# Kernel tuning notes

Measured on AMD Instinct MI355X. Metric: run time of the kernel, lower is better.

## Reference

```python
import jax, jax.numpy as jnp
import numpy as np

B = 32768
INPUT_DIM = 2048
D = 2
HIDDEN = 128
V = 20          # output_dim (number of heads)
P = 6           # n_corr_params
R = 10          # r_lora = min(V // 2, 10)


def setup_inputs() -> dict:
    key = jax.random.key(0)
    ks = jax.random.split(key, 12)

    def lin(k, fan_in, shape):
        bound = 1.0 / np.sqrt(fan_in)
        return jax.random.uniform(k, shape, jnp.float32, -bound, bound)

    x = jax.random.normal(ks[0], (B, INPUT_DIM), jnp.float32)
    # encoder: Linear(input_dim, hidden) -> ReLU -> (Dropout=id) -> Linear(hidden, d)
    We1 = lin(ks[1], INPUT_DIM, (INPUT_DIM, HIDDEN))
    be1 = lin(ks[2], INPUT_DIM, (HIDDEN,))
    We2 = lin(ks[3], HIDDEN, (HIDDEN, D))
    be2 = lin(ks[4], HIDDEN, (D,))
    # 20 heads, each Linear(d, hidden) -> ReLU -> Linear(hidden, 6) -> Tanh,
    # stacked into batched weight tensors.
    W1 = lin(ks[5], D, (V, D, HIDDEN))
    b1 = lin(ks[6], D, (V, HIDDEN))
    W2 = lin(ks[7], HIDDEN, (V, HIDDEN, P))
    b2 = lin(ks[8], HIDDEN, (V, P))
    # LoRA params
    lora_A = jax.random.normal(ks[9], (D, R), jnp.float32) * 0.01
    lora_B = jax.random.normal(ks[10], (R, V * P), jnp.float32) * 0.01
    return {"x": x, "We1": We1, "be1": be1, "We2": We2, "be2": be2,
            "W1": W1, "b1": b1, "W2": W2, "b2": b2,
            "lora_A": lora_A, "lora_B": lora_B}


def reference(x, We1, be1, We2, be2, W1, b1, W2, b2, lora_A, lora_B):
    # encoder (nonlinear reduction; dropout is identity in eval)
    z = jax.nn.relu(x @ We1 + be1) @ We2 + be2            # [B, D]
    # all 20 heads as batched GEMMs
    h = jax.nn.relu(jnp.einsum('bd,vdh->bvh', z, W1) + b1)  # [B, V, HIDDEN]
    heads = jnp.tanh(jnp.einsum('bvh,vhp->bvp', h, W2) + b2)  # [B, V, P]
    # LoRA contribution, then outer tanh (note: double tanh, faithful to source)
    lora = (z @ lora_A @ lora_B).reshape(-1, V, P)         # [B, V, P]
    out = jnp.tanh(heads + 0.15 * lora)
    return (out, z)
```

## Files before the change

### kernel.cpp

```cpp
#include <hip/hip_runtime.h>
#include <hip/hip_bf16.h>
#include <cstdint>
#include <cstddef>

#define BDIM   32768
#define KDIM   2048
#define NDIM   128
#define VHEADS 20
#define PDIM   6
#define RLORA  10

#define BK      64
#define NCHUNK  (KDIM / BK)
#define OUT_ELEMS   (BDIM * VHEADS * PDIM)
#define WS_W_BYTES  (KDIM * NDIM * 2)

typedef __attribute__((ext_vector_type(8))) __bf16 bf16x8;
typedef __attribute__((ext_vector_type(4))) float f32x4;
typedef __attribute__((ext_vector_type(2))) float f32x2;
typedef __attribute__((ext_vector_type(4))) unsigned int u32x4;

union FragU { bf16x8 b; u32x4 u; };

__device__ __forceinline__ unsigned int cvt_pk_bf16(float lo, float hi) {
  unsigned int r;
  asm("v_cvt_pk_bf16_f32 %0, %1, %2" : "=v"(r) : "v"(lo), "v"(hi));
  return r;
}

__device__ __forceinline__ void gload_lds16(const void* g, void* l) {
  __builtin_amdgcn_global_load_lds(
      (const __attribute__((address_space(1))) void*)(g),
      (__attribute__((address_space(3))) void*)(l), 16, 0, 0);
}

__device__ __forceinline__ float fast_tanh(float x) {
  float ax = fabsf(x);
  float e  = __expf(-2.0f * ax);
  float t  = __fdividef(1.0f - e, 1.0f + e);
  return copysignf(t, x);
}

#define SBAR() __builtin_amdgcn_sched_barrier(0)

__global__ __launch_bounds__(256)
void k0_pack(const float* __restrict__ We1,
             const float* __restrict__ lA,
             const float* __restrict__ lB,
             unsigned short* __restrict__ wsw,
             float* __restrict__ wsM) {
  if (blockIdx.x == 128) {
    int t = threadIdx.x;
    if (t < 2 * VHEADS * PDIM) {
      int d  = t / (VHEADS * PDIM);
      int vp = t - d * (VHEADS * PDIM);
      float s = 0.f;
#pragma unroll
      for (int r = 0; r < RLORA; ++r)
        s = fmaf(lA[d * RLORA + r], lB[r * (VHEADS * PDIM) + vp], s);
      wsM[t] = s;
    }
    return;
  }
  int t    = blockIdx.x * 256 + threadIdx.x;
  int lane = t & 63;
  int blk  = t >> 6;
  int ks   = blk & 1;
  int nt   = (blk >> 1) & 7;
  int c    = blk >> 4;
  int n    = nt * 16 + (lane & 15);
  int kb   = c * 64 + ks * 32 + (lane >> 4) * 8;

  unsigned int u[4];
#pragma unroll
  for (int q = 0; q < 4; ++q) {
    float f0 = We1[(size_t)(kb + 2 * q + 0) * NDIM + n];
    float f1 = We1[(size_t)(kb + 2 * q + 1) * NDIM + n];
    __hip_bfloat16 h0 = __float2bfloat16(f0);
    __hip_bfloat16 h1 = __float2bfloat16(f1);
    u[q] = (unsigned int)*reinterpret_cast<unsigned short*>(&h0) |
           ((unsigned int)*reinterpret_cast<unsigned short*>(&h1) << 16);
  }
  *reinterpret_cast<u32x4*>(wsw + (size_t)t * 8) = u32x4{u[0], u[1], u[2], u[3]};
}

__global__ __launch_bounds__(512, 4)
void k1_fused(const float* __restrict__ x,
              const unsigned short* __restrict__ wp,
              const float* __restrict__ be1,
              const float* __restrict__ We2,
              const float* __restrict__ be2,
              const float* __restrict__ W1,
              const float* __restrict__ b1,
              const float* __restrict__ W2,
              const float* __restrict__ b2,
              const float* __restrict__ M,
              float* __restrict__ out,
              float* __restrict__ zout) {
  __shared__ char A0_[16384] __attribute__((aligned(16)));
  __shared__ char A1_[16384] __attribute__((aligned(16)));
  __shared__ char B0_[16384] __attribute__((aligned(16)));
  __shared__ char B1_[16384] __attribute__((aligned(16)));
  __shared__ float zpart2[64][2][2];
  __shared__ float zsh[64][2];

  const int tid  = threadIdx.x;
  const int lane = tid & 63;
  const int wv   = tid >> 6;
  const int wr   = wv & 3;
  const int wc   = wv >> 2;
  const int l15  = lane & 15;
  const int kgrp = lane >> 4;
  const int blk  = blockIdx.x;

  f32x4 acc[4];
#pragma unroll
  for (int i = 0; i < 4; ++i) acc[i] = f32x4{0.f, 0.f, 0.f, 0.f};

  auto STAGE = [&](char* Ad, char* Bd, int c) {
#pragma unroll
    for (int q = 0; q < 2; ++q) {
      int s = tid + q * 512;
      int row = s >> 4;
      int g = (s & 15) ^ (row & 7);
      const float* asrc = x + (size_t)(blk * 64 + row) * KDIM + c * BK + g * 4;
      gload_lds16(asrc, Ad + s * 16);
    }
#pragma unroll
    for (int q = 0; q < 2; ++q) {
      gload_lds16((const char*)wp + (size_t)c * 16384 + q * 8192 + tid * 16,
                  Bd + q * 8192 + tid * 16);
    }
  };

  auto COMPUTE = [&](const char* Ad, const char* Bd) {
    const int row = wr * 16 + l15;
    const char* abase = Ad + row * 256;
    const int rx = (row & 7) << 4;
    f32x4 A0 = *(const f32x4*)(abase + (((kgrp * 2 + 0) << 4) ^ rx));
    f32x4 A1 = *(const f32x4*)(abase + (((kgrp * 2 + 1) << 4) ^ rx));
    f32x4 A2 = *(const f32x4*)(abase + 128 + (((kgrp * 2 + 0) << 4) ^ rx));
    f32x4 A3 = *(const f32x4*)(abase + 128 + (((kgrp * 2 + 1) << 4) ^ rx));
    FragU a0, a1;
    a0.u = u32x4{cvt_pk_bf16(A0.x, A0.y), cvt_pk_bf16(A0.z, A0.w),
                 cvt_pk_bf16(A1.x, A1.y), cvt_pk_bf16(A1.z, A1.w)};
    a1.u = u32x4{cvt_pk_bf16(A2.x, A2.y), cvt_pk_bf16(A2.z, A2.w),
                 cvt_pk_bf16(A3.x, A3.y), cvt_pk_bf16(A3.z, A3.w)};
    const char* bbase = Bd + lane * 16;
#pragma unroll
    for (int nt = 0; nt < 4; ++nt) {
      FragU b0, b1;
      b0.u = *(const u32x4*)(bbase + ((wc * 4 + nt) * 2 + 0) * 1024);
      b1.u = *(const u32x4*)(bbase + ((wc * 4 + nt) * 2 + 1) * 1024);
      acc[nt] = __builtin_amdgcn_mfma_f32_16x16x32_bf16(a0.b, b0.b, acc[nt], 0, 0, 0);
      acc[nt] = __builtin_amdgcn_mfma_f32_16x16x32_bf16(a1.b, b1.b, acc[nt], 0, 0, 0);
    }
  };

  STAGE(A0_, B0_, 0);
  STAGE(A1_, B1_, 1);

#pragma unroll 1
  for (int cc = 0; cc < NCHUNK / 2 - 1; ++cc) {
    asm volatile("s_waitcnt vmcnt(4)" ::: "memory");
    SBAR();
    __builtin_amdgcn_s_barrier();
    COMPUTE(A0_, B0_);
    __builtin_amdgcn_s_barrier();
    SBAR();
    STAGE(A0_, B0_, 2 * cc + 2);
    asm volatile("s_waitcnt vmcnt(4)" ::: "memory");
    SBAR();
    __builtin_amdgcn_s_barrier();
    COMPUTE(A1_, B1_);
    __builtin_amdgcn_s_barrier();
    SBAR();
    STAGE(A1_, B1_, 2 * cc + 3);
  }
  asm volatile("s_waitcnt vmcnt(4)" ::: "memory");
  SBAR();
  __builtin_amdgcn_s_barrier();
  COMPUTE(A0_, B0_);
  asm volatile("s_waitcnt vmcnt(0)" ::: "memory");
  SBAR();
  __builtin_amdgcn_s_barrier();
  COMPUTE(A1_, B1_);

  float part[4][2];
#pragma unroll
  for (int j = 0; j < 4; ++j) { part[j][0] = 0.f; part[j][1] = 0.f; }
#pragma unroll
  for (int nt = 0; nt < 4; ++nt) {
    int col = (wc * 4 + nt) * 16 + l15;
    float bb = be1[col];
    float w0 = We2[col * 2 + 0];
    float w1 = We2[col * 2 + 1];
#pragma unroll
    for (int j = 0; j < 4; ++j) {
      float h = acc[nt][j] + bb;
      h = h > 0.f ? h : 0.f;
      part[j][0] = fmaf(h, w0, part[j][0]);
      part[j][1] = fmaf(h, w1, part[j][1]);
    }
  }
#pragma unroll
  for (int m = 1; m < 16; m <<= 1) {
#pragma unroll
    for (int j = 0; j < 4; ++j) {
      part[j][0] += __shfl_xor(part[j][0], m, 64);
      part[j][1] += __shfl_xor(part[j][1], m, 64);
    }
  }
  if (l15 == 0) {
#pragma unroll
    for (int j = 0; j < 4; ++j) {
      int rl = wr * 16 + kgrp * 4 + j;
      zpart2[rl][wc][0] = part[j][0];
      zpart2[rl][wc][1] = part[j][1];
    }
  }
  __syncthreads();
  if (tid < 64) {
    float s0 = zpart2[tid][0][0] + zpart2[tid][1][0] + be2[0];
    float s1 = zpart2[tid][0][1] + zpart2[tid][1][1] + be2[1];
    zsh[tid][0] = s0;
    zsh[tid][1] = s1;
    f32x2 zz = {s0, s1};
    *(f32x2*)(zout + (size_t)(blk * 64 + tid) * 2) = zz;
  }
  __syncthreads();

  const int wvu = __builtin_amdgcn_readfirstlane(wv);
  float z0 = zsh[lane][0];
  float z1 = zsh[lane][1];
  float* orow = out + (size_t)(blk * 64 + lane) * (VHEADS * PDIM);

  auto head = [&](int v) {
    const float* w1a = W1 + (size_t)(v * 2 + 0) * NDIM;
    const float* w1b = W1 + (size_t)(v * 2 + 1) * NDIM;
    const float* bb1 = b1 + (size_t)v * NDIM;
    const float* w2  = W2 + (size_t)v * NDIM * PDIM;

    float p[6] = {0.f, 0.f, 0.f, 0.f, 0.f, 0.f};
#pragma unroll 4
    for (int h = 0; h < NDIM; ++h) {
      float hv = fmaf(z0, w1a[h], fmaf(z1, w1b[h], bb1[h]));
      hv = hv > 0.f ? hv : 0.f;
#pragma unroll
      for (int j = 0; j < 6; ++j) p[j] = fmaf(hv, w2[h * 6 + j], p[j]);
    }
    float o[6];
#pragma unroll
    for (int j = 0; j < 6; ++j) {
      float t1 = fast_tanh(p[j] + b2[v * PDIM + j]);
      float lo = fmaf(z0, M[v * PDIM + j], z1 * M[VHEADS * PDIM + v * PDIM + j]);
      o[j] = fast_tanh(fmaf(0.15f, lo, t1));
    }
    float* op = orow + v * PDIM;
    f32x2 o01 = {o[0], o[1]};
    f32x2 o23 = {o[2], o[3]};
    f32x2 o45 = {o[4], o[5]};
    __builtin_nontemporal_store(o01, (f32x2*)(op + 0));
    __builtin_nontemporal_store(o23, (f32x2*)(op + 2));
    __builtin_nontemporal_store(o45, (f32x2*)(op + 4));
  };

  head(wvu);
  head(wvu + 8);
  if (wvu < 4) head(wvu + 16);
}

extern "C" void kernel_launch(void* const* d_in, const int* in_sizes, int n_in,
                              void* d_out, int out_size, void* d_ws, size_t ws_size,
                              hipStream_t stream) {
  const float* x   = (const float*)d_in[0];
  const float* We1 = (const float*)d_in[1];
  const float* be1 = (const float*)d_in[2];
  const float* We2 = (const float*)d_in[3];
  const float* be2 = (const float*)d_in[4];
  const float* W1  = (const float*)d_in[5];
  const float* b1  = (const float*)d_in[6];
  const float* W2  = (const float*)d_in[7];
  const float* b2  = (const float*)d_in[8];
  const float* lA  = (const float*)d_in[9];
  const float* lB  = (const float*)d_in[10];

  float* out  = (float*)d_out;
  float* zout = out + OUT_ELEMS;
  unsigned short* wsw = (unsigned short*)d_ws;
  float* wsM = (float*)((char*)d_ws + WS_W_BYTES);

  hipLaunchKernelGGL(k0_pack, dim3(129), dim3(256), 0, stream,
                     We1, lA, lB, wsw, wsM);
  hipLaunchKernelGGL(k1_fused, dim3(BDIM / 64), dim3(512), 0, stream,
                     x, wsw, be1, We2, be2, W1, b1, W2, b2, wsM, out, zout);
}
```

Before: 95.87 us.

## Load packed weight fragments directly into registers instead of staging through LDS

The bf16 weight tile is no longer staged through shared memory. Each wave now loads its B fragments straight from global memory into double-buffered registers with inline-asm dwordx4 loads, and the vmcnt waits are adjusted to match. This removes the LDS round trip and halves LDS usage, which could allow more resident blocks. In exchange each wave separately re-fetches B that was previously shared across the block, register pressure rises, and correctness depends on hand-counted vmcnt values with inline asm the compiler cannot track.

```diff
diff --git a/kernel.cpp b/kernel.cpp
--- a/kernel.cpp
+++ b/kernel.cpp
@@ -42,6 +42,9 @@
 }
 
 #define SBAR() __builtin_amdgcn_sched_barrier(0)
+#define GL16(dst, addr, OFFSTR) \
+  asm volatile("global_load_dwordx4 %0, %1, off offset:" OFFSTR \
+               : "=v"(dst) : "v"(addr))
 
 __global__ __launch_bounds__(256)
 void k0_pack(const float* __restrict__ We1,
@@ -99,8 +102,6 @@
               float* __restrict__ zout) {
   __shared__ char A0_[16384] __attribute__((aligned(16)));
   __shared__ char A1_[16384] __attribute__((aligned(16)));
-  __shared__ char B0_[16384] __attribute__((aligned(16)));
-  __shared__ char B1_[16384] __attribute__((aligned(16)));
   __shared__ float zpart2[64][2][2];
   __shared__ float zsh[64][2];
 
@@ -113,11 +114,13 @@
   const int kgrp = lane >> 4;
   const int blk  = blockIdx.x;
 
+  const char* bwave = (const char*)wp + wc * 8192 + lane * 16 + 4096;
+
   f32x4 acc[4];
 #pragma unroll
   for (int i = 0; i < 4; ++i) acc[i] = f32x4{0.f, 0.f, 0.f, 0.f};
 
-  auto STAGE = [&](char* Ad, char* Bd, int c) {
+  auto STAGE_A = [&](char* Ad, int c) {
 #pragma unroll
     for (int q = 0; q < 2; ++q) {
       int s = tid + q * 512;
@@ -126,14 +129,22 @@
       const float* asrc = x + (size_t)(blk * 64 + row) * KDIM + c * BK + g * 4;
       gload_lds16(asrc, Ad + s * 16);
     }
-#pragma unroll
-    for (int q = 0; q < 2; ++q) {
-      gload_lds16((const char*)wp + (size_t)c * 16384 + q * 8192 + tid * 16,
-                  Bd + q * 8192 + tid * 16);
-    }
   };
 
-  auto COMPUTE = [&](const char* Ad, const char* Bd) {
+  FragU bE[8], bO[8];
+  auto LOADB = [&](FragU* B, int c) {
+    const char* p = bwave + (size_t)c * 16384;
+    GL16(B[0].u, p, "-4096");
+    GL16(B[1].u, p, "-3072");
+    GL16(B[2].u, p, "-2048");
+    GL16(B[3].u, p, "-1024");
+    GL16(B[4].u, p, "0");
+    GL16(B[5].u, p, "1024");
+    GL16(B[6].u, p, "2048");
+    GL16(B[7].u, p, "3072");
+  };
+
+  auto COMPUTE = [&](const char* Ad, const FragU* B) {
     const int row = wr * 16 + l15;
     const char* abase = Ad + row * 256;
     const int rx = (row & 7) << 4;
@@ -146,45 +157,48 @@
                  cvt_pk_bf16(A1.x, A1.y), cvt_pk_bf16(A1.z, A1.w)};
     a1.u = u32x4{cvt_pk_bf16(A2.x, A2.y), cvt_pk_bf16(A2.z, A2.w),
                  cvt_pk_bf16(A3.x, A3.y), cvt_pk_bf16(A3.z, A3.w)};
-    const char* bbase = Bd + lane * 16;
-#pragma unroll
-    for (int nt = 0; nt < 4; ++nt) {
-      FragU b0, b1;
-      b0.u = *(const u32x4*)(bbase + ((wc * 4 + nt) * 2 + 0) * 1024);
-      b1.u = *(const u32x4*)(bbase + ((wc * 4 + nt) * 2 + 1) * 1024);
-      acc[nt] = __builtin_amdgcn_mfma_f32_16x16x32_bf16(a0.b, b0.b, acc[nt], 0, 0, 0);
-      acc[nt] = __builtin_amdgcn_mfma_f32_16x16x32_bf16(a1.b, b1.b, acc[nt], 0, 0, 0);
-    }
+    acc[0] = __builtin_amdgcn_mfma_f32_16x16x32_bf16(a0.b, B[0].b, acc[0], 0, 0, 0);
+    acc[0] = __builtin_amdgcn_mfma_f32_16x16x32_bf16(a1.b, B[1].b, acc[0], 0, 0, 0);
+    acc[1] = __builtin_amdgcn_mfma_f32_16x16x32_bf16(a0.b, B[2].b, acc[1], 0, 0, 0);
+    acc[1] = __builtin_amdgcn_mfma_f32_16x16x32_bf16(a1.b, B[3].b, acc[1], 0, 0, 0);
+    acc[2] = __builtin_amdgcn_mfma_f32_16x16x32_bf16(a0.b, B[4].b, acc[2], 0, 0, 0);
+    acc[2] = __builtin_amdgcn_mfma_f32_16x16x32_bf16(a1.b, B[5].b, acc[2], 0, 0, 0);
+    acc[3] = __builtin_amdgcn_mfma_f32_16x16x32_bf16(a0.b, B[6].b, acc[3], 0, 0, 0);
+    acc[3] = __builtin_amdgcn_mfma_f32_16x16x32_bf16(a1.b, B[7].b, acc[3], 0, 0, 0);
   };
 
-  STAGE(A0_, B0_, 0);
-  STAGE(A1_, B1_, 1);
+  STAGE_A(A0_, 0);
+  LOADB(bE, 0);
+  STAGE_A(A1_, 1);
+  LOADB(bO, 1);
 
 #pragma unroll 1
   for (int cc = 0; cc < NCHUNK / 2 - 1; ++cc) {
-    asm volatile("s_waitcnt vmcnt(4)" ::: "memory");
+    asm volatile("s_waitcnt vmcnt(10)" ::: "memory");
     SBAR();
     __builtin_amdgcn_s_barrier();
-    COMPUTE(A0_, B0_);
+    COMPUTE(A0_, bE);
     __builtin_amdgcn_s_barrier();
     SBAR();
-    STAGE(A0_, B0_, 2 * cc + 2);
-    asm volatile("s_waitcnt vmcnt(4)" ::: "memory");
+    STAGE_A(A0_, 2 * cc + 2);
+    LOADB(bE, 2 * cc + 2);
+    asm volatile("s_waitcnt vmcnt(10)" ::: "memory");
     SBAR();
     __builtin_amdgcn_s_barrier();
-    COMPUTE(A1_, B1_);
+    COMPUTE(A1_, bO);
     __builtin_amdgcn_s_barrier();
     SBAR();
-    STAGE(A1_, B1_, 2 * cc + 3);
-  }
-  asm volatile("s_waitcnt vmcnt(4)" ::: "memory");
+    STAGE_A(A1_, 2 * cc + 3);
+    LOADB(bO, 2 * cc + 3);
+  }
+  asm volatile("s_waitcnt vmcnt(10)" ::: "memory");
   SBAR();
   __builtin_amdgcn_s_barrier();
-  COMPUTE(A0_, B0_);
+  COMPUTE(A0_, bE);
   asm volatile("s_waitcnt vmcnt(0)" ::: "memory");
   SBAR();
   __builtin_amdgcn_s_barrier();
-  COMPUTE(A1_, B1_);
+  COMPUTE(A1_, bO);
 
   float part[4][2];
 #pragma unroll
```

Measured after the change: 99.55 us. 1.04x slower.

## Enlarge row tile to 128 with 1024-thread blocks and single-buffered B

Applied to the files above, without the earlier changes.

Doubles the rows each block handles (64 to 128) by running 16 waves per block. Each staged We1 tile is now reused across twice as many rows, and the grid is halved. The B (weight) tile drops from double to single buffering, and the B and A loads are reordered so that the vmcnt waits still cover the data in flight. The head epilogue is remapped so each group of 128 threads handles one row set per head slot. The risk is lower occupancy, since one larger block now takes more LDS and registers, and the B loads are now serialized behind the barriers.

```diff
diff --git a/kernel.cpp b/kernel.cpp
--- a/kernel.cpp
+++ b/kernel.cpp
@@ -10,6 +10,7 @@
 #define PDIM   6
 #define RLORA  10
 
+#define BM      128
 #define BK      64
 #define NCHUNK  (KDIM / BK)
 #define OUT_ELEMS   (BDIM * VHEADS * PDIM)
@@ -84,7 +85,7 @@
   *reinterpret_cast<u32x4*>(wsw + (size_t)t * 8) = u32x4{u[0], u[1], u[2], u[3]};
 }
 
-__global__ __launch_bounds__(512, 4)
+__global__ __launch_bounds__(1024, 4)
 void k1_fused(const float* __restrict__ x,
               const unsigned short* __restrict__ wp,
               const float* __restrict__ be1,
@@ -97,18 +98,17 @@
               const float* __restrict__ M,
               float* __restrict__ out,
               float* __restrict__ zout) {
-  __shared__ char A0_[16384] __attribute__((aligned(16)));
-  __shared__ char A1_[16384] __attribute__((aligned(16)));
+  __shared__ char A0_[32768] __attribute__((aligned(16)));
+  __shared__ char A1_[32768] __attribute__((aligned(16)));
   __shared__ char B0_[16384] __attribute__((aligned(16)));
-  __shared__ char B1_[16384] __attribute__((aligned(16)));
-  __shared__ float zpart2[64][2][2];
-  __shared__ float zsh[64][2];
+  __shared__ float zpart2[128][2][2];
+  __shared__ float zsh[128][2];
 
   const int tid  = threadIdx.x;
   const int lane = tid & 63;
   const int wv   = tid >> 6;
-  const int wr   = wv & 3;
-  const int wc   = wv >> 2;
+  const int wr   = wv & 7;
+  const int wc   = wv >> 3;
   const int l15  = lane & 15;
   const int kgrp = lane >> 4;
   const int blk  = blockIdx.x;
@@ -117,23 +117,22 @@
 #pragma unroll
   for (int i = 0; i < 4; ++i) acc[i] = f32x4{0.f, 0.f, 0.f, 0.f};
 
-  auto STAGE = [&](char* Ad, char* Bd, int c) {
+  auto STAGE_A = [&](char* Ad, int c) {
 #pragma unroll
     for (int q = 0; q < 2; ++q) {
-      int s = tid + q * 512;
+      int s = tid + q * 1024;
       int row = s >> 4;
       int g = (s & 15) ^ (row & 7);
-      const float* asrc = x + (size_t)(blk * 64 + row) * KDIM + c * BK + g * 4;
+      const float* asrc = x + (size_t)(blk * BM + row) * KDIM + c * BK + g * 4;
       gload_lds16(asrc, Ad + s * 16);
     }
-#pragma unroll
-    for (int q = 0; q < 2; ++q) {
-      gload_lds16((const char*)wp + (size_t)c * 16384 + q * 8192 + tid * 16,
-                  Bd + q * 8192 + tid * 16);
-    }
-  };
-
-  auto COMPUTE = [&](const char* Ad, const char* Bd) {
+  };
+  auto STAGE_B = [&](int c) {
+    gload_lds16((const char*)wp + (size_t)c * 16384 + tid * 16,
+                B0_ + tid * 16);
+  };
+
+  auto COMPUTE = [&](const char* Ad) {
     const int row = wr * 16 + l15;
     const char* abase = Ad + row * 256;
     const int rx = (row & 7) << 4;
@@ -146,7 +145,7 @@
                  cvt_pk_bf16(A1.x, A1.y), cvt_pk_bf16(A1.z, A1.w)};
     a1.u = u32x4{cvt_pk_bf16(A2.x, A2.y), cvt_pk_bf16(A2.z, A2.w),
                  cvt_pk_bf16(A3.x, A3.y), cvt_pk_bf16(A3.z, A3.w)};
-    const char* bbase = Bd + lane * 16;
+    const char* bbase = B0_ + lane * 16;
 #pragma unroll
     for (int nt = 0; nt < 4; ++nt) {
       FragU b0, b1;
@@ -157,34 +156,35 @@
     }
   };
 
-  STAGE(A0_, B0_, 0);
-  STAGE(A1_, B1_, 1);
+  STAGE_B(0);
+  STAGE_A(A0_, 0);
+  STAGE_A(A1_, 1);
 
 #pragma unroll 1
-  for (int cc = 0; cc < NCHUNK / 2 - 1; ++cc) {
-    asm volatile("s_waitcnt vmcnt(4)" ::: "memory");
-    SBAR();
-    __builtin_amdgcn_s_barrier();
-    COMPUTE(A0_, B0_);
-    __builtin_amdgcn_s_barrier();
-    SBAR();
-    STAGE(A0_, B0_, 2 * cc + 2);
-    asm volatile("s_waitcnt vmcnt(4)" ::: "memory");
-    SBAR();
-    __builtin_amdgcn_s_barrier();
-    COMPUTE(A1_, B1_);
-    __builtin_amdgcn_s_barrier();
-    SBAR();
-    STAGE(A1_, B1_, 2 * cc + 3);
-  }
-  asm volatile("s_waitcnt vmcnt(4)" ::: "memory");
-  SBAR();
-  __builtin_amdgcn_s_barrier();
-  COMPUTE(A0_, B0_);
-  asm volatile("s_waitcnt vmcnt(0)" ::: "memory");
-  SBAR();
-  __builtin_amdgcn_s_barrier();
-  COMPUTE(A1_, B1_);
+  for (int cc = 0; cc < NCHUNK / 2; ++cc) {
+    asm volatile("s_waitcnt vmcnt(2)" ::: "memory");
+    SBAR();
+    __builtin_amdgcn_s_barrier();
+    COMPUTE(A0_);
+    __builtin_amdgcn_s_barrier();
+    SBAR();
+    STAGE_B(2 * cc + 1);
+    if (cc + 1 < NCHUNK / 2) STAGE_A(A0_, 2 * cc + 2);
+    if (cc + 1 < NCHUNK / 2) {
+      asm volatile("s_waitcnt vmcnt(2)" ::: "memory");
+    } else {
+      asm volatile("s_waitcnt vmcnt(0)" ::: "memory");
+    }
+    SBAR();
+    __builtin_amdgcn_s_barrier();
+    COMPUTE(A1_);
+    __builtin_amdgcn_s_barrier();
+    SBAR();
+    if (cc + 1 < NCHUNK / 2) {
+      STAGE_B(2 * cc + 2);
+      STAGE_A(A1_, 2 * cc + 3);
+    }
+  }
 
   float part[4][2];
 #pragma unroll
@@ -220,20 +220,21 @@
     }
   }
   __syncthreads();
-  if (tid < 64) {
+  if (tid < BM) {
     float s0 = zpart2[tid][0][0] + zpart2[tid][1][0] + be2[0];
     float s1 = zpart2[tid][0][1] + zpart2[tid][1][1] + be2[1];
     zsh[tid][0] = s0;
     zsh[tid][1] = s1;
     f32x2 zz = {s0, s1};
-    *(f32x2*)(zout + (size_t)(blk * 64 + tid) * 2) = zz;
+    *(f32x2*)(zout + (size_t)(blk * BM + tid) * 2) = zz;
   }
   __syncthreads();
 
-  const int wvu = __builtin_amdgcn_readfirstlane(wv);
-  float z0 = zsh[lane][0];
-  float z1 = zsh[lane][1];
-  float* orow = out + (size_t)(blk * 64 + lane) * (VHEADS * PDIM);
+  const int srow = tid & 127;
+  const int slot = tid >> 7;
+  float z0 = zsh[srow][0];
+  float z1 = zsh[srow][1];
+  float* orow = out + (size_t)(blk * BM + srow) * (VHEADS * PDIM);
 
   auto head = [&](int v) {
     const float* w1a = W1 + (size_t)(v * 2 + 0) * NDIM;
@@ -265,9 +266,9 @@
     __builtin_nontemporal_store(o45, (f32x2*)(op + 4));
   };
 
-  head(wvu);
-  head(wvu + 8);
-  if (wvu < 4) head(wvu + 16);
+  head(slot);
+  head(slot + 8);
+  if (slot < 4) head(slot + 16);
 }
 
 extern "C" void kernel_launch(void* const* d_in, const int* in_sizes, int n_in,
@@ -292,6 +293,6 @@
 
   hipLaunchKernelGGL(k0_pack, dim3(129), dim3(256), 0, stream,
                      We1, lA, lB, wsw, wsM);
-  hipLaunchKernelGGL(k1_fused, dim3(BDIM / 64), dim3(512), 0, stream,
+  hipLaunchKernelGGL(k1_fused, dim3(BDIM / BM), dim3(1024), 0, stream,
                      x, wsw, be1, We2, be2, W1, b1, W2, b2, wsM, out, zout);
 }
```

Measured after the change: 147.9 us. 1.54x slower.
